# Kernel optimization log

Hardware: AMD Instinct MI355X
Metric: run time of the kernel (lower is better)

Reference implementation:

```python
import jax, jax.numpy as jnp
import numpy as np

HIDDEN = 1024

def setup_inputs() -> dict:
    key = jax.random.key(0)
    k1, k2, k3 = jax.random.split(key, 3)
    X = jax.random.normal(k1, (4, 4096, HIDDEN), dtype=jnp.float32)
    # nn.Linear(hidden, 3*hidden): weight [3h, h], bias [3h]
    W = jax.random.normal(k2, (3 * HIDDEN, HIDDEN), dtype=jnp.float32) / np.sqrt(HIDDEN)
    b = jax.random.normal(k3, (3 * HIDDEN,), dtype=jnp.float32) * 0.01
    return {"X": X, "W": W, "b": b}

def reference(X, W, b):
    h = X.shape[-1]
    QKV = jnp.einsum('bsh,oh->bso', X, W) + b  # [B,S,3h]
    Q, K, V = jnp.split(QKV, 3, axis=-1)
    scores = jnp.einsum('bqh,bkh->bqk', Q, K) / jnp.sqrt(jnp.float32(h))
    attn = jax.nn.softmax(scores, axis=-1)
    return jnp.einsum('bqk,bkh->bqh', attn, V)
```

## Files before the change

kernel.cpp:

```cpp
#include <hip/hip_runtime.h>
#include <hip/hip_bf16.h>

typedef unsigned short u16;
typedef _Float16 f16x8 __attribute__((ext_vector_type(8)));
typedef _Float16 f16x2 __attribute__((ext_vector_type(2)));
typedef float f32x4 __attribute__((ext_vector_type(4)));

#if __has_builtin(__builtin_amdgcn_exp2f)
#define EXP2F(x) __builtin_amdgcn_exp2f(x)
#else
#define EXP2F(x) exp2f(x)
#endif
#define FA_C32 0.045084220027780106f

__device__ __forceinline__ f32x4 mfma16h(f16x8 a, f16x8 b, f32x4 c) {
  return __builtin_amdgcn_mfma_f32_16x16x32_f16(a, b, c, 0, 0, 0);
}
__device__ __forceinline__ unsigned pk2h(float a, float b) {
  union { _Float16 h[2]; unsigned u; } x;
  x.h[0] = (_Float16)a; x.h[1] = (_Float16)b;
  return x.u;
}
__device__ __forceinline__ u16 h1(float a) {
  union { _Float16 h; u16 u; } x; x.h = (_Float16)a; return x.u;
}

#if __has_builtin(__builtin_amdgcn_fdot2)
__device__ __forceinline__ float fdot2_(f16x2 a, f16x2 b, float c) {
  return __builtin_amdgcn_fdot2(a, b, c, false);
}
#else
__device__ __forceinline__ float fdot2_(f16x2 a, f16x2 b, float c) {
  return c + (float)a[0] * (float)b[0] + (float)a[1] * (float)b[1];
}
#endif

typedef __attribute__((address_space(1))) const unsigned int gas_u32;
typedef __attribute__((address_space(3))) unsigned int las_u32;
__device__ __forceinline__ void gl_lds16(const u16* g, u16* l) {
  __builtin_amdgcn_global_load_lds((gas_u32*)g, (las_u32*)l, 16, 0, 0);
}

__global__ __launch_bounds__(256) void cast_f16_k(const float* __restrict__ src,
                                                  u16* __restrict__ dst, int n8) {
  int i = blockIdx.x * 256 + threadIdx.x;
  if (i >= n8) return;
  const float4* s4 = (const float4*)src;
  float4 a = s4[i * 2], b = s4[i * 2 + 1];
  uint4 o;
  o.x = pk2h(a.x, a.y); o.y = pk2h(a.z, a.w);
  o.z = pk2h(b.x, b.y); o.w = pk2h(b.z, b.w);
  ((uint4*)dst)[i] = o;
}

template <int K_, int EPI>
__global__ __launch_bounds__(512, 2) void gemm8p(
    const u16* __restrict__ A, const u16* __restrict__ B,
    const float* __restrict__ bias, u16* __restrict__ D0, u16* __restrict__ D1,
    u16* __restrict__ D2, float* __restrict__ Df, const int ldc,
    const size_t strA, const size_t strB, const size_t strC) {
  constexpr int NT = K_ / 64;
  static_assert(NT >= 4 && (NT % 2) == 0, "need even NT >= 4");
  __shared__ __align__(16) u16 As[2][2][128 * 64];
  __shared__ __align__(16) u16 Bs[2][2][128 * 64];
  __shared__ float lds_l[256];

  const int tid = threadIdx.x, lane = tid & 63, wid = tid >> 6;
  const int l15 = lane & 15, lhi = lane >> 4;
  const int m0 = blockIdx.x * 256, n0 = blockIdx.y * 256;
  const int wm = wid >> 2, wn = wid & 3;
  const u16* Ag = A + (size_t)blockIdx.z * strA;
  const u16* Bg = B + (size_t)blockIdx.z * strB;

  const int srow8 = lane >> 3;
  const int sblk = (lane & 7) ^ srow8;

#define STAGE_Q(BUF, G, GROW0, ST)                                        \
  gl_lds16((G) + (size_t)((GROW0) + wid * 8 + srow8) * K_ +               \
               (ST) * 64 + sblk * 8,                                      \
           (BUF) + (wid * 8) * 64)

#define BAR()                                                             \
  asm volatile("" ::: "memory");                                          \
  __builtin_amdgcn_s_barrier();                                           \
  asm volatile("" ::: "memory")

#define LGKM0()                                                           \
  asm volatile("s_waitcnt lgkmcnt(0)" ::: "memory");                      \
  __builtin_amdgcn_sched_barrier(0)

#define SB0() __builtin_amdgcn_sched_barrier(0)
#define VMC8() asm volatile("s_waitcnt vmcnt(8)" ::: "memory")
#define VMC0() asm volatile("s_waitcnt vmcnt(0)" ::: "memory")

#define RD_A(DST, PB, MH)                                                 \
  _Pragma("unroll") for (int mf = 0; mf < 4; ++mf)                        \
  _Pragma("unroll") for (int ks = 0; ks < 2; ++ks)                        \
    DST[mf][ks] = *(const f16x8*)((PB) + ((MH) * 64 + mf * 16 + l15) * 64 \
                                  + (((ks * 4 + lhi) ^ (l15 & 7)) * 8));

#define RD_B(DST, PB, BO, NH)                                             \
  _Pragma("unroll") for (int nf = 0; nf < 2; ++nf)                        \
  _Pragma("unroll") for (int ks = 0; ks < 2; ++ks)                        \
    DST[nf][ks] = *(const f16x8*)((PB) + ((BO) + (NH) * 32 + nf * 16 + l15) * 64 \
                                  + (((ks * 4 + lhi) ^ (l15 & 7)) * 8));

#define MM(AV, BV, MB, NB2)                                               \
  __builtin_amdgcn_s_setprio(1);                                          \
  _Pragma("unroll") for (int mf = 0; mf < 4; ++mf)                        \
  _Pragma("unroll") for (int nf = 0; nf < 2; ++nf)                        \
  _Pragma("unroll") for (int ks = 0; ks < 2; ++ks)                        \
    acc[(MB) * 4 + mf][(NB2) * 2 + nf] =                                  \
        mfma16h(AV[mf][ks], BV[nf][ks], acc[(MB) * 4 + mf][(NB2) * 2 + nf]); \
  __builtin_amdgcn_s_setprio(0);

#define SUMA(FR, MH8)                                                     \
  if (EPI == 1 && wn == 0) {                                              \
    _Pragma("unroll") for (int mf = 0; mf < 4; ++mf)                      \
    _Pragma("unroll") for (int ks = 0; ks < 2; ++ks) {                    \
      const f16x2* _pr = (const f16x2*)&FR[mf][ks];                       \
      _Pragma("unroll") for (int j = 0; j < 4; ++j)                       \
        lsa[MH8][mf] = fdot2_(_pr[j], ones2, lsa[MH8][mf]);               \
    }                                                                     \
  }

  f32x4 acc[8][4];
#pragma unroll
  for (int i = 0; i < 8; ++i)
#pragma unroll
    for (int j = 0; j < 4; ++j) acc[i][j] = 0.f;

  float lsa[2][4];
#pragma unroll
  for (int i = 0; i < 2; ++i)
#pragma unroll
    for (int j = 0; j < 4; ++j) lsa[i][j] = 0.f;
  const f16x2 ones2 = {(_Float16)1.0f, (_Float16)1.0f};

  const int bofs = (wn & 1) * 64;

#define STAGE_TILE(DB, T)                                                 \
  STAGE_Q(&As[DB][0][0],    Ag, m0,       T);                             \
  STAGE_Q(&As[DB][0][4096], Ag, m0 + 64,  T);                             \
  STAGE_Q(&As[DB][1][0],    Ag, m0 + 128, T);                             \
  STAGE_Q(&As[DB][1][4096], Ag, m0 + 192, T);                             \
  STAGE_Q(&Bs[DB][0][0],    Bg, n0,       T);                             \
  STAGE_Q(&Bs[DB][0][4096], Bg, n0 + 64,  T);                             \
  STAGE_Q(&Bs[DB][1][0],    Bg, n0 + 128, T);                             \
  STAGE_Q(&Bs[DB][1][4096], Bg, n0 + 192, T)

  STAGE_TILE(0, 0);
  STAGE_TILE(1, 1);
  VMC8();
  BAR();

#define PHASES4(DB, TN, PRE)                                              \
  {                                                                       \
    const u16* Apb = &As[DB][wm][0];                                      \
    const u16* Bpb = &Bs[DB][wn >> 1][0];                                 \
                                             \
    RD_A(a0, Apb, 0);                                                     \
    RD_B(b0, Bpb, bofs, 0);                                               \
    BAR();                                                                \
    LGKM0();                                                              \
    MM(a0, b0, 0, 0);                                                     \
    SUMA(a0, 0);                                                          \
    SB0();                                                                \
    BAR();                                                                \
       \
    RD_B(b1, Bpb, bofs, 1);                                               \
    if (PRE) { STAGE_Q(&As[DB][0][0], Ag, m0,       TN);                  \
               STAGE_Q(&As[DB][1][0], Ag, m0 + 128, TN); }                \
    BAR();                                                                \
    LGKM0();                                                              \
    MM(a0, b1, 0, 1);                                                     \
    SB0();                                                                \
    BAR();                                                                \
     \
    RD_A(a1, Apb, 1);                                                     \
    if (PRE) { STAGE_Q(&Bs[DB][0][0],    Bg, n0,       TN);               \
               STAGE_Q(&Bs[DB][0][4096], Bg, n0 + 64,  TN);               \
               STAGE_Q(&Bs[DB][1][0],    Bg, n0 + 128, TN);               \
               STAGE_Q(&Bs[DB][1][4096], Bg, n0 + 192, TN); }             \
    BAR();                                                                \
    LGKM0();                                                              \
    MM(a1, b1, 1, 1);                                                     \
    SUMA(a1, 1);                                                          \
    SB0();                                                                \
    BAR();                                                                \
     \
    if (PRE) { STAGE_Q(&As[DB][0][4096], Ag, m0 + 64,  TN);               \
               STAGE_Q(&As[DB][1][4096], Ag, m0 + 192, TN); }             \
    BAR();                                                                \
    LGKM0();                                                              \
    MM(a1, b0, 1, 0);                                                     \
    SB0();                                                                \
    if (PRE) { VMC8(); } else { VMC0(); }                                 \
    BAR();                                                                \
  }

  for (int it = 0; it < NT / 2; ++it) {
    const int t0 = 2 * it;
    const bool pre = (t0 + 2 < NT);
    f16x8 a0[4][2], a1[4][2], b0[2][2], b1[2][2];
    PHASES4(0, t0 + 2, pre)
    PHASES4(1, t0 + 3, pre)
  }
#undef PHASES4
#undef STAGE_TILE
#undef STAGE_Q
#undef BAR
#undef LGKM0
#undef SB0
#undef VMC8
#undef VMC0
#undef RD_A
#undef RD_B
#undef MM
#undef SUMA

  if (EPI == 2) {
    float bv[4];
#pragma unroll
    for (int cf = 0; cf < 4; ++cf) bv[cf] = bias[n0 + wn * 64 + cf * 16 + l15];
    const int region = n0 >> 10;
    const int ncol0 = (n0 & 1023) + wn * 64;
    if (region < 2) {
      u16* dst = region ? D1 : D0;
#pragma unroll
      for (int rf = 0; rf < 8; ++rf) {
        const int m = m0 + wm * 128 + rf * 16 + lhi * 4;
#pragma unroll
        for (int r = 0; r < 4; ++r)
#pragma unroll
          for (int cf = 0; cf < 4; ++cf)
            dst[(size_t)(m + r) * 1024 + ncol0 + cf * 16 + l15] = h1(acc[rf][cf][r] + bv[cf]);
      }
    } else {
#pragma unroll
      for (int rf = 0; rf < 8; ++rf) {
        const int m = m0 + wm * 128 + rf * 16 + lhi * 4;
        const int bb = m >> 12, s = m & 4095;
#pragma unroll
        for (int cf = 0; cf < 4; ++cf) {
          const int dcol = ncol0 + cf * 16 + l15;
          uint2 v;
          v.x = pk2h(acc[rf][cf][0] + bv[cf], acc[rf][cf][1] + bv[cf]);
          v.y = pk2h(acc[rf][cf][2] + bv[cf], acc[rf][cf][3] + bv[cf]);
          *(uint2*)&D2[(size_t)(bb * 1024 + dcol) * 4096 + s] = v;
        }
      }
    }
  } else if (EPI == 0) {
#pragma unroll
    for (int rf = 0; rf < 8; ++rf) {
      const int m = m0 + wm * 128 + rf * 16 + lhi * 4;
#pragma unroll
      for (int r = 0; r < 4; ++r)
#pragma unroll
        for (int cf = 0; cf < 4; ++cf) {
          const int n = n0 + wn * 64 + cf * 16 + l15;
          float p = fminf(EXP2F(acc[rf][cf][r] * FA_C32), 60000.f);
          D0[(size_t)blockIdx.z * strC + (size_t)(m + r) * ldc + n] = h1(p);
        }
    }
  } else {
    if (wn == 0) {
#pragma unroll
      for (int mh = 0; mh < 2; ++mh)
#pragma unroll
        for (int mf = 0; mf < 4; ++mf) {
          float s = lsa[mh][mf];
          s += __shfl_xor(s, 16, 64);
          s += __shfl_xor(s, 32, 64);
          if (lhi == 0) lds_l[wm * 128 + mh * 64 + mf * 16 + l15] = s;
        }
    }
    __syncthreads();
#pragma unroll
    for (int rf = 0; rf < 8; ++rf) {
      const int m = m0 + wm * 128 + rf * 16 + lhi * 4;
#pragma unroll
      for (int r = 0; r < 4; ++r) {
        const float li = 1.0f / lds_l[wm * 128 + rf * 16 + lhi * 4 + r];
#pragma unroll
        for (int cf = 0; cf < 4; ++cf) {
          const int n = n0 + wn * 64 + cf * 16 + l15;
          Df[(size_t)blockIdx.z * strC + (size_t)(m + r) * ldc + n] = acc[rf][cf][r] * li;
        }
      }
    }
  }
}

extern "C" void kernel_launch(void* const* d_in, const int* in_sizes, int n_in,
                              void* d_out, int out_size, void* d_ws, size_t ws_size,
                              hipStream_t stream) {
  const float* X = (const float*)d_in[0];
  const float* W = (const float*)d_in[1];
  const float* b = (const float*)d_in[2];
  float* out = (float*)d_out;
  char* ws = (char*)d_ws;

  const size_t SB = (size_t)4096 * 4096 * 2;
  const size_t QB = (size_t)4096 * 1024 * 2;
  const size_t WFB = (size_t)3072 * 1024 * 2;
  int NB = 1;
  if (ws_size >= 4 * SB + WFB + 12 * QB) NB = 4;
  else if (ws_size >= 2 * SB + WFB + 12 * QB) NB = 2;

  u16* S  = (u16*)(ws);
  u16* Xf = (u16*)(ws);
  u16* Wf = (u16*)(ws + (size_t)NB * SB);
  u16* Qf = (u16*)(ws + (size_t)NB * SB + WFB);
  u16* Kf = (u16*)(ws + (size_t)NB * SB + WFB + 4 * QB);
  u16* Vt = (u16*)(ws + (size_t)NB * SB + WFB + 8 * QB);

  cast_f16_k<<<8192, 256, 0, stream>>>(X, Xf, 16777216 / 8);
  cast_f16_k<<<1536, 256, 0, stream>>>(W, Wf, 3145728 / 8);

  gemm8p<1024, 2><<<dim3(64, 12, 1), 512, 0, stream>>>(
      Xf, Wf, b, Qf, Kf, Vt, nullptr, 0, 0, 0, 0);

  const size_t strQ = (size_t)4096 * 1024;
  const size_t strS = (size_t)4096 * 4096;
  const size_t strV = (size_t)1024 * 4096;
  for (int g = 0; g < 4; g += NB) {
    const u16* Qg = Qf + (size_t)g * strQ;
    const u16* Kg = Kf + (size_t)g * strQ;
    const u16* Vg = Vt + (size_t)g * strV;
    float* Og = out + (size_t)g * strQ;
    gemm8p<1024, 0><<<dim3(16, 16, NB), 512, 0, stream>>>(
        Qg, Kg, nullptr, S, nullptr, nullptr, nullptr, 4096, strQ, strQ, strS);
    gemm8p<4096, 1><<<dim3(16, 4, NB), 512, 0, stream>>>(
        S, Vg, nullptr, nullptr, nullptr, nullptr, Og, 1024, strS, strV, strQ);
  }
}
```

Measured before the change: 417.4 us.

## Restructure GEMM main loop into 3-phase pipeline with earlier A-half prefetch

```diff
diff --git a/kernel.cpp b/kernel.cpp
--- a/kernel.cpp
+++ b/kernel.cpp
@@ -54,7 +54,7 @@
 }
 
 template <int K_, int EPI>
-__global__ __launch_bounds__(512, 2) void gemm8p(
+__global__ __launch_bounds__(512, 1) void gemm8p(
     const u16* __restrict__ A, const u16* __restrict__ B,
     const float* __restrict__ bias, u16* __restrict__ D0, u16* __restrict__ D1,
     u16* __restrict__ D2, float* __restrict__ Df, const int ldc,
@@ -90,7 +90,7 @@
   __builtin_amdgcn_sched_barrier(0)
 
 #define SB0() __builtin_amdgcn_sched_barrier(0)
-#define VMC8() asm volatile("s_waitcnt vmcnt(8)" ::: "memory")
+#define VMC6() asm volatile("s_waitcnt vmcnt(6)" ::: "memory")
 #define VMC0() asm volatile("s_waitcnt vmcnt(0)" ::: "memory")
 
 #define RD_A(DST, PB, MH)                                                 \
@@ -139,80 +139,76 @@
 
   const int bofs = (wn & 1) * 64;
 
-#define STAGE_TILE(DB, T)                                                 \
-  STAGE_Q(&As[DB][0][0],    Ag, m0,       T);                             \
-  STAGE_Q(&As[DB][0][4096], Ag, m0 + 64,  T);                             \
-  STAGE_Q(&As[DB][1][0],    Ag, m0 + 128, T);                             \
-  STAGE_Q(&As[DB][1][4096], Ag, m0 + 192, T);                             \
-  STAGE_Q(&Bs[DB][0][0],    Bg, n0,       T);                             \
-  STAGE_Q(&Bs[DB][0][4096], Bg, n0 + 64,  T);                             \
-  STAGE_Q(&Bs[DB][1][0],    Bg, n0 + 128, T);                             \
-  STAGE_Q(&Bs[DB][1][4096], Bg, n0 + 192, T)
-
-  STAGE_TILE(0, 0);
-  STAGE_TILE(1, 1);
-  VMC8();
+  STAGE_Q(&As[0][0][0],    Ag, m0,       0);
+  STAGE_Q(&As[0][0][4096], Ag, m0 + 64,  0);
+  STAGE_Q(&As[0][1][0],    Ag, m0 + 128, 0);
+  STAGE_Q(&As[0][1][4096], Ag, m0 + 192, 0);
+  STAGE_Q(&Bs[0][0][0],    Bg, n0,       0);
+  STAGE_Q(&Bs[0][0][4096], Bg, n0 + 64,  0);
+  STAGE_Q(&Bs[0][1][0],    Bg, n0 + 128, 0);
+  STAGE_Q(&Bs[0][1][4096], Bg, n0 + 192, 0);
+  STAGE_Q(&As[1][0][0],    Ag, m0,       1);
+  STAGE_Q(&As[1][1][0],    Ag, m0 + 128, 1);
+  STAGE_Q(&Bs[1][0][0],    Bg, n0,       1);
+  STAGE_Q(&Bs[1][0][4096], Bg, n0 + 64,  1);
+  STAGE_Q(&Bs[1][1][0],    Bg, n0 + 128, 1);
+  STAGE_Q(&Bs[1][1][4096], Bg, n0 + 192, 1);
+  VMC6();
   BAR();
 
-#define PHASES4(DB, TN, PRE)                                              \
-  {                                                                       \
-    const u16* Apb = &As[DB][wm][0];                                      \
-    const u16* Bpb = &Bs[DB][wn >> 1][0];                                 \
-                                             \
-    RD_A(a0, Apb, 0);                                                     \
-    RD_B(b0, Bpb, bofs, 0);                                               \
-    BAR();                                                                \
-    LGKM0();                                                              \
-    MM(a0, b0, 0, 0);                                                     \
-    SUMA(a0, 0);                                                          \
-    SB0();                                                                \
-    BAR();                                                                \
-       \
-    RD_B(b1, Bpb, bofs, 1);                                               \
-    if (PRE) { STAGE_Q(&As[DB][0][0], Ag, m0,       TN);                  \
-               STAGE_Q(&As[DB][1][0], Ag, m0 + 128, TN); }                \
-    BAR();                                                                \
-    LGKM0();                                                              \
-    MM(a0, b1, 0, 1);                                                     \
-    SB0();                                                                \
-    BAR();                                                                \
-     \
-    RD_A(a1, Apb, 1);                                                     \
-    if (PRE) { STAGE_Q(&Bs[DB][0][0],    Bg, n0,       TN);               \
-               STAGE_Q(&Bs[DB][0][4096], Bg, n0 + 64,  TN);               \
-               STAGE_Q(&Bs[DB][1][0],    Bg, n0 + 128, TN);               \
-               STAGE_Q(&Bs[DB][1][4096], Bg, n0 + 192, TN); }             \
-    BAR();                                                                \
-    LGKM0();                                                              \
-    MM(a1, b1, 1, 1);                                                     \
-    SUMA(a1, 1);                                                          \
-    SB0();                                                                \
-    BAR();                                                                \
-     \
-    if (PRE) { STAGE_Q(&As[DB][0][4096], Ag, m0 + 64,  TN);               \
-               STAGE_Q(&As[DB][1][4096], Ag, m0 + 192, TN); }             \
-    BAR();                                                                \
-    LGKM0();                                                              \
-    MM(a1, b0, 1, 0);                                                     \
-    SB0();                                                                \
-    if (PRE) { VMC8(); } else { VMC0(); }                                 \
-    BAR();                                                                \
+#pragma unroll 2
+  for (int u = 0; u < NT; ++u) {
+    const int d = u & 1;
+    const u16* Apb = &As[d][wm][0];
+    const u16* Bpb = &Bs[d][wn >> 1][0];
+    f16x8 a0[4][2], a1[4][2], b0[2][2], b1[2][2];
+
+    RD_A(a0, Apb, 0);
+    RD_B(b0, Bpb, bofs, 0);
+    if (u + 1 < NT) {
+      STAGE_Q(&As[d ^ 1][0][4096], Ag, m0 + 64,  u + 1);
+      STAGE_Q(&As[d ^ 1][1][4096], Ag, m0 + 192, u + 1);
+    }
+    BAR();
+    LGKM0();
+    MM(a0, b0, 0, 0);
+    SUMA(a0, 0);
+    SB0();
+    BAR();
+
+    RD_B(b1, Bpb, bofs, 1);
+    if (u + 2 < NT) {
+      STAGE_Q(&As[d][0][0], Ag, m0,       u + 2);
+      STAGE_Q(&As[d][1][0], Ag, m0 + 128, u + 2);
+    }
+    BAR();
+    LGKM0();
+    MM(a0, b1, 0, 1);
+    SB0();
+    BAR();
+
+    RD_A(a1, Apb, 1);
+    if (u + 2 < NT) {
+      STAGE_Q(&Bs[d][0][0],    Bg, n0,       u + 2);
+      STAGE_Q(&Bs[d][0][4096], Bg, n0 + 64,  u + 2);
+      STAGE_Q(&Bs[d][1][0],    Bg, n0 + 128, u + 2);
+      STAGE_Q(&Bs[d][1][4096], Bg, n0 + 192, u + 2);
+    }
+    BAR();
+    LGKM0();
+    MM(a1, b1, 1, 1);
+    SUMA(a1, 1);
+    MM(a1, b0, 1, 0);
+    SB0();
+    if (u + 2 < NT) { VMC6(); }
+    else if (u + 2 == NT) { VMC0(); }
+    BAR();
   }
-
-  for (int it = 0; it < NT / 2; ++it) {
-    const int t0 = 2 * it;
-    const bool pre = (t0 + 2 < NT);
-    f16x8 a0[4][2], a1[4][2], b0[2][2], b1[2][2];
-    PHASES4(0, t0 + 2, pre)
-    PHASES4(1, t0 + 3, pre)
-  }
-#undef PHASES4
-#undef STAGE_TILE
 #undef STAGE_Q
 #undef BAR
 #undef LGKM0
 #undef SB0
-#undef VMC8
+#undef VMC6
 #undef VMC0
 #undef RD_A
 #undef RD_B
```

New measurement: 391.8 us. 1.07x faster.
